# Kernel tuning notes

Hardware: AMD Instinct MI355X
Metric: run time of the kernel (lower is better)

## Reference

```python
import jax, jax.numpy as jnp
import numpy as np

B = 262144
NUM_PLAYERS = 450
EMBED = 8


def _lin(x, w, b):
    return x @ w + b


def setup_inputs() -> dict:
    key = jax.random.key(0)
    ks = jax.random.split(key, 32)
    # state: 73 continuous features + 5 player ids stored as floats
    cont = jax.random.normal(ks[0], (B, 73), dtype=jnp.float32)
    pids = jax.random.randint(ks[1], (B, 5), 0, NUM_PLAYERS).astype(jnp.float32)
    state = jnp.concatenate([cont, pids], axis=1)

    def w(k, shape, fan_in):
        return jax.random.normal(k, shape, dtype=jnp.float32) * (2.0 / fan_in) ** 0.5

    base_in = 13 + EMBED + 32      # ctx(21) + pooled defender phi(32) = 53
    pass_in = 32 + base_in         # tm_phi(32) + base(53) = 85? no: 32+53=85 -> wait
    pass_in = 32 + (13 + EMBED) + 32  # tm_phi + ctx + def_pooled = 32+21+32 = 85
    # Match torch: pass_input = 32 + ctx_dim + 32 where ctx_dim = 13+embed = 21 -> 85?
    # torch: ctx_dim = 13 + embed_dim = 21; base_input = ctx_dim + 32 = 53; pass_input = 32 + ctx_dim + 32 = 85.
    # BUT forward concatenates [tm_phi, ctx, def_pooled] = 32 + 21 + 32 = 85. Consistent.
    pass_in = 85
    return {
        "state": state,
        "emb": jax.random.normal(ks[2], (NUM_PLAYERS, EMBED), dtype=jnp.float32),
        "wd1": w(ks[3], (4, 32), 4),   "bd1": jnp.zeros((32,), jnp.float32),
        "wd2": w(ks[4], (32, 32), 32), "bd2": jnp.zeros((32,), jnp.float32),
        "wt1": w(ks[5], (10 + EMBED, 32), 18), "bt1": jnp.zeros((32,), jnp.float32),
        "wt2": w(ks[6], (32, 32), 32),         "bt2": jnp.zeros((32,), jnp.float32),
        "wv1": w(ks[7], (base_in, 64), base_in), "bv1": jnp.zeros((64,), jnp.float32),
        "wv2": w(ks[8], (64, 32), 64),           "bv2": jnp.zeros((32,), jnp.float32),
        "wv3": w(ks[9], (32, 1), 32),            "bv3": jnp.zeros((1,), jnp.float32),
        "ws1": w(ks[10], (base_in, 32), base_in), "bs1": jnp.zeros((32,), jnp.float32),
        "ws2": w(ks[11], (32, 1), 32),            "bs2": jnp.zeros((1,), jnp.float32),
        "wp1": w(ks[12], (pass_in, 64), pass_in), "bp1": jnp.zeros((64,), jnp.float32),
        "wp2": w(ks[13], (64, 16), 64),           "bp2": jnp.zeros((16,), jnp.float32),
        "wp3": w(ks[14], (16, 1), 16),            "bp3": jnp.zeros((1,), jnp.float32),
    }


def reference(state, emb, wd1, bd1, wd2, bd2, wt1, bt1, wt2, bt2,
              wv1, bv1, wv2, bv2, wv3, bv3, ws1, bs1, ws2, bs2,
              wp1, bp1, wp2, bp2, wp3, bp3):
    b = state.shape[0]
    context = state[:, :11]
    tm_open = state[:, 11:15]
    tm_fg = state[:, 15:19]
    tm_dist = state[:, 19:23]
    def_pos = state[:, 23:33].reshape(b, 5, 2)
    tm_pos = state[:, 33:41].reshape(b, 4, 2)
    bh_vel = state[:, 41:43]
    def_vel = state[:, 43:53].reshape(b, 5, 2)
    tm_vel = state[:, 53:61].reshape(b, 4, 2)
    tm_lane_min = state[:, 61:65]
    tm_corridor = state[:, 65:69]
    tm_pass_dist = state[:, 69:73]

    pids = jnp.clip(state[:, 73:78].astype(jnp.int32), 0, NUM_PLAYERS - 1)
    bh_embed = emb[pids[:, 0]]            # [b, E]
    tm_embeds = emb[pids[:, 1:5]]         # [b, 4, E]

    # batched defender phi over 5 entities: [b,5,4] -> [b,5,32]
    d_feat = jnp.concatenate([def_pos, def_vel], axis=-1)
    d_h = jax.nn.relu(jax.nn.relu(d_feat @ wd1 + bd1) @ wd2 + bd2)
    def_pooled = d_h.mean(axis=1)         # [b, 32]

    ctx = jnp.concatenate([context, bh_vel, bh_embed], axis=1)   # [b, 21]
    base = jnp.concatenate([ctx, def_pooled], axis=1)            # [b, 53]

    value = jax.nn.relu(jax.nn.relu(base @ wv1 + bv1) @ wv2 + bv2) @ wv3 + bv3  # [b,1]
    a_shoot = jax.nn.relu(base @ ws1 + bs1) @ ws2 + bs2                          # [b,1]

    # batched teammate phi over 4 entities: [b,4,18] -> [b,4,32]
    t_feat = jnp.concatenate([
        tm_pos, tm_vel,
        tm_open[:, :, None], tm_fg[:, :, None], tm_dist[:, :, None],
        tm_lane_min[:, :, None], tm_corridor[:, :, None], tm_pass_dist[:, :, None],
        tm_embeds,
    ], axis=-1)
    tm_phi = jax.nn.relu(jax.nn.relu(t_feat @ wt1 + bt1) @ wt2 + bt2)  # [b,4,32]

    base_b = jnp.broadcast_to(base[:, None, :], (b, 4, base.shape[1]))
    p_in = jnp.concatenate([tm_phi, base_b], axis=-1)                   # [b,4,85]
    a_pass = (jax.nn.relu(jax.nn.relu(p_in @ wp1 + bp1) @ wp2 + bp2) @ wp3 + bp3)[..., 0]  # [b,4]
    a_pass = a_pass - a_pass.mean(axis=1, keepdims=True)

    q_shoot = value + a_shoot          # [b,1]
    q_passes = value + a_pass          # [b,4]
    return jnp.concatenate([q_shoot, q_passes], axis=1)
```

## Files before the change

kernel.cpp:

```cpp
#include <hip/hip_runtime.h>
#include <hip/hip_bf16.h>

#define THREADS 512

typedef short bf16x8 __attribute__((ext_vector_type(8)));
typedef float f32x4 __attribute__((ext_vector_type(4)));

union FragU { unsigned u[4]; bf16x8 v; };

__device__ __forceinline__ void split8(const float* x, FragU& hi, FragU& lo) {
#pragma unroll
    for (int i = 0; i < 4; ++i) {
        float a = x[2 * i], b = x[2 * i + 1];
        __hip_bfloat162 h2 = __float22bfloat162_rn(make_float2(a, b));
        float ra = __bfloat162float(h2.x), rb = __bfloat162float(h2.y);
        __hip_bfloat162 l2 = __float22bfloat162_rn(make_float2(a - ra, b - rb));
        unsigned hu, lu;
        __builtin_memcpy(&hu, &h2, 4);
        __builtin_memcpy(&lu, &l2, 4);
        hi.u[i] = hu; lo.u[i] = lu;
    }
}

__device__ __forceinline__ f32x4 mm3(const FragU& ah, const FragU& al,
                                     const FragU& bh, const FragU& bl, f32x4 acc) {
    acc = __builtin_amdgcn_mfma_f32_16x16x32_bf16(al.v, bh.v, acc, 0, 0, 0);
    acc = __builtin_amdgcn_mfma_f32_16x16x32_bf16(ah.v, bl.v, acc, 0, 0, 0);
    acc = __builtin_amdgcn_mfma_f32_16x16x32_bf16(ah.v, bh.v, acc, 0, 0, 0);
    return acc;
}

__device__ __forceinline__ void load_pair(const uint4* __restrict__ ws, int pair, int lane,
                                          FragU& hi, FragU& lo) {
    uint4 a = ws[pair * 128 + lane];
    uint4 b = ws[pair * 128 + 64 + lane];
    hi.u[0] = a.x; hi.u[1] = a.y; hi.u[2] = a.z; hi.u[3] = a.w;
    lo.u[0] = b.x; lo.u[1] = b.y; lo.u[2] = b.z; lo.u[3] = b.w;
}

__device__ __forceinline__ void buildA(const float* buf, int stride, int m, int kf, int lane,
                                       FragU& hi, FragU& lo) {
    const float* p = buf + (m * 16 + (lane & 15)) * stride + kf * 32 + ((lane >> 4) * 8);
    float x[8];
    *reinterpret_cast<float4*>(&x[0]) = *reinterpret_cast<const float4*>(p);
    *reinterpret_cast<float4*>(&x[4]) = *reinterpret_cast<const float4*>(p + 4);
    split8(x, hi, lo);
}

__device__ __forceinline__ void storeC(float* buf, int stride, int m, int nf, int lane, f32x4 c) {
    float* p = buf + (((lane >> 4) * 4) + m * 16) * stride + nf * 16 + (lane & 15);
    p[0] = c[0]; p[stride] = c[1]; p[2 * stride] = c[2]; p[3 * stride] = c[3];
}

#define PB_D2  0
#define PB_T1  2
#define PB_T2  4
#define PB_P1T 6
#define PB_P1B 10
#define PB_P2  18
#define PB_V1  20
#define PB_V2  28
#define PB_S1  32
#define WS_BYTES (36 * 2048)

__global__ __launch_bounds__(64)
void prep_weights(const float* __restrict__ wd2, const float* __restrict__ wt1,
                  const float* __restrict__ wt2, const float* __restrict__ wp1,
                  const float* __restrict__ wp2, const float* __restrict__ wv1,
                  const float* __restrict__ wv2, const float* __restrict__ ws1,
                  uint4* __restrict__ wsout) {
    const int pair = blockIdx.x;
    const int lane = threadIdx.x;
    const int base_[10]  = {0, 2, 4, 6, 10, 18, 20, 28, 32, 36};
    const int kreal_[9]  = {32, 18, 32, 32, 53, 64, 53, 64, 53};
    const int n_[9]      = {32, 32, 32, 64, 64, 16, 64, 32, 32};
    const int nfc_[9]    = {2, 2, 2, 4, 4, 1, 4, 2, 2};
    const int roff_[9]   = {0, 0, 0, 0, 32, 0, 0, 0, 0};
    int g = 0;
    while (g < 8 && pair >= base_[g + 1]) ++g;
    const int local = pair - base_[g];
    const int kf = local / nfc_[g];
    const int nfi = local % nfc_[g];
    const float* W = (g == 0) ? wd2 : (g == 1) ? wt1 : (g == 2) ? wt2 :
                     (g == 3 || g == 4) ? wp1 : (g == 5) ? wp2 :
                     (g == 6) ? wv1 : (g == 7) ? wv2 : ws1;
    const int N = n_[g];
    float x[8];
#pragma unroll
    for (int j = 0; j < 8; ++j) {
        const int k = kf * 32 + (lane >> 4) * 8 + j;
        const int n = nfi * 16 + (lane & 15);
        x[j] = (k < kreal_[g]) ? W[(roff_[g] + k) * N + n] : 0.0f;
    }
    FragU hi, lo;
    split8(x, hi, lo);
    wsout[pair * 128 + lane]      = make_uint4(hi.u[0], hi.u[1], hi.u[2], hi.u[3]);
    wsout[pair * 128 + 64 + lane] = make_uint4(lo.u[0], lo.u[1], lo.u[2], lo.u[3]);
}

#define SB 68
#define SS 36
#define WAVE_F 4608

__global__ __launch_bounds__(THREADS, 2)
void dueling_mfma(const float* __restrict__ state, const float* __restrict__ emb,
                  const float* __restrict__ wd1, const float* __restrict__ bd1,
                  const float* __restrict__ bd2, const float* __restrict__ bt1,
                  const float* __restrict__ bt2, const float* __restrict__ bv1,
                  const float* __restrict__ bv2, const float* __restrict__ wv3,
                  const float* __restrict__ bv3, const float* __restrict__ bs1,
                  const float* __restrict__ ws2, const float* __restrict__ bs2,
                  const float* __restrict__ bp1, const float* __restrict__ bp2,
                  const float* __restrict__ wp3,
                  const uint4* __restrict__ ws, float* __restrict__ out, int nrows) {
    __shared__ float smem[8 * WAVE_F];
    const int lane = threadIdx.x & 63;
    const int wave = threadIdx.x >> 6;
    const int row = blockIdx.x * THREADS + wave * 64 + lane;
    const float* __restrict__ s = state + (long long)row * 78;

    float* BASE = smem + wave * WAVE_F;
    float* BUFA = BASE;
    float* BUFB = BASE + 64 * SS;
    float* HST  = BASE + 24;
    const int c16 = lane & 15;

#pragma unroll
    for (int i = 0; i < 17; ++i)
        *reinterpret_cast<float4*>(BASE + lane * SB + i * 4) = make_float4(0.f, 0.f, 0.f, 0.f);

    {
        int pid0 = (int)s[73];
        pid0 = pid0 < 0 ? 0 : (pid0 > 449 ? 449 : pid0);
        const float4 e0 = *(const float4*)(emb + pid0 * 8);
        const float4 e1 = *(const float4*)(emb + pid0 * 8 + 4);
        float* bp = BASE + lane * SB;
        *reinterpret_cast<float4*>(bp +  0) = make_float4(s[0], s[1], s[2], s[3]);
        *reinterpret_cast<float4*>(bp +  4) = make_float4(s[4], s[5], s[6], s[7]);
        *reinterpret_cast<float4*>(bp +  8) = make_float4(s[8], s[9], s[10], s[41]);
        *reinterpret_cast<float4*>(bp + 12) = make_float4(s[42], e0.x, e0.y, e0.z);
        *reinterpret_cast<float4*>(bp + 16) = make_float4(e0.w, e1.x, e1.y, e1.z);
        bp[20] = e1.w;
    }

    float pool[4][2][4];
#pragma unroll
    for (int m = 0; m < 4; ++m)
#pragma unroll
        for (int nf = 0; nf < 2; ++nf)
#pragma unroll
            for (int q = 0; q < 4; ++q) pool[m][nf][q] = 0.0f;

#pragma unroll 1
    for (int p = 0; p < 5; ++p) {
        const float f0 = s[23 + 2 * p], f1 = s[24 + 2 * p];
        const float f2 = s[43 + 2 * p], f3 = s[44 + 2 * p];
#pragma unroll
        for (int i = 0; i < 8; ++i) {
            const float4 b4 = *(const float4*)(bd1 + i * 4);
            const float4 w0 = *(const float4*)(wd1 + 0 * 32 + i * 4);
            const float4 w1 = *(const float4*)(wd1 + 1 * 32 + i * 4);
            const float4 w2 = *(const float4*)(wd1 + 2 * 32 + i * 4);
            const float4 w3 = *(const float4*)(wd1 + 3 * 32 + i * 4);
            float4 hv;
            hv.x = fmaxf(fmaf(f0, w0.x, fmaf(f1, w1.x, fmaf(f2, w2.x, fmaf(f3, w3.x, b4.x)))), 0.f);
            hv.y = fmaxf(fmaf(f0, w0.y, fmaf(f1, w1.y, fmaf(f2, w2.y, fmaf(f3, w3.y, b4.y)))), 0.f);
            hv.z = fmaxf(fmaf(f0, w0.z, fmaf(f1, w1.z, fmaf(f2, w2.z, fmaf(f3, w3.z, b4.z)))), 0.f);
            hv.w = fmaxf(fmaf(f0, w0.w, fmaf(f1, w1.w, fmaf(f2, w2.w, fmaf(f3, w3.w, b4.w)))), 0.f);
            *reinterpret_cast<float4*>(BASE + lane * SB + 24 + i * 4) = hv;
        }

        FragU ah[4], al[4];
#pragma unroll
        for (int m = 0; m < 4; ++m) buildA(HST, SB, m, 0, lane, ah[m], al[m]);
#pragma unroll
        for (int nf = 0; nf < 2; ++nf) {
            FragU bh, bl; load_pair(ws, PB_D2 + nf, lane, bh, bl);
            const float bias = bd2[nf * 16 + c16];
#pragma unroll
            for (int m = 0; m < 4; ++m) {
                f32x4 acc = {bias, bias, bias, bias};
                acc = mm3(ah[m], al[m], bh, bl, acc);
#pragma unroll
                for (int q = 0; q < 4; ++q) pool[m][nf][q] += fmaxf(acc[q], 0.0f);
            }
        }
    }
    BASE[lane * SB + 53] = 0.0f;
    BASE[lane * SB + 54] = 0.0f;
    BASE[lane * SB + 55] = 0.0f;
#pragma unroll
    for (int m = 0; m < 4; ++m)
#pragma unroll
        for (int nf = 0; nf < 2; ++nf)
#pragma unroll
            for (int q = 0; q < 4; ++q)
                BASE[((lane >> 4) * 4 + q + m * 16) * SB + 21 + nf * 16 + c16] =
                    pool[m][nf][q] * 0.2f;

    FragU Xh[4][2], Xl[4][2];
#pragma unroll
    for (int m = 0; m < 4; ++m)
#pragma unroll
        for (int kf = 0; kf < 2; ++kf)
            buildA(BASE, SB, m, kf, lane, Xh[m][kf], Xl[m][kf]);

    float v2acc[4][2][4];
#pragma unroll
    for (int m = 0; m < 4; ++m)
#pragma unroll
        for (int nf = 0; nf < 2; ++nf) {
            const float b = bv2[nf * 16 + c16];
#pragma unroll
            for (int q = 0; q < 4; ++q) v2acc[m][nf][q] = b;
        }
#pragma unroll 1
    for (int half = 0; half < 2; ++half) {
#pragma unroll
        for (int nfl = 0; nfl < 2; ++nfl) {
            const int ng = half * 2 + nfl;
            FragU b0h, b0l, b1h, b1l;
            load_pair(ws, PB_V1 + ng, lane, b0h, b0l);
            load_pair(ws, PB_V1 + 4 + ng, lane, b1h, b1l);
            const float bias = bv1[ng * 16 + c16];
#pragma unroll
            for (int m = 0; m < 4; ++m) {
                f32x4 acc = {bias, bias, bias, bias};
                acc = mm3(Xh[m][0], Xl[m][0], b0h, b0l, acc);
                acc = mm3(Xh[m][1], Xl[m][1], b1h, b1l, acc);
#pragma unroll
                for (int q = 0; q < 4; ++q) acc[q] = fmaxf(acc[q], 0.0f);
                storeC(BUFA, SS, m, nfl, lane, acc);
            }
        }
        FragU ah[4], al[4];
#pragma unroll
        for (int m = 0; m < 4; ++m) buildA(BUFA, SS, m, 0, lane, ah[m], al[m]);
#pragma unroll
        for (int nf = 0; nf < 2; ++nf) {
            FragU bh, bl; load_pair(ws, PB_V2 + half * 2 + nf, lane, bh, bl);
#pragma unroll
            for (int m = 0; m < 4; ++m) {
                f32x4 acc = {v2acc[m][nf][0], v2acc[m][nf][1], v2acc[m][nf][2], v2acc[m][nf][3]};
                acc = mm3(ah[m], al[m], bh, bl, acc);
#pragma unroll
                for (int q = 0; q < 4; ++q) v2acc[m][nf][q] = acc[q];
            }
        }
    }
#pragma unroll
    for (int m = 0; m < 4; ++m)
#pragma unroll
        for (int nf = 0; nf < 2; ++nf) {
            f32x4 r = {fmaxf(v2acc[m][nf][0], 0.f), fmaxf(v2acc[m][nf][1], 0.f),
                       fmaxf(v2acc[m][nf][2], 0.f), fmaxf(v2acc[m][nf][3], 0.f)};
            storeC(BUFA, SS, m, nf, lane, r);
        }
    float value = bv3[0];
#pragma unroll
    for (int c4 = 0; c4 < 8; ++c4) {
        float4 v = *reinterpret_cast<const float4*>(BUFA + lane * SS + c4 * 4);
        value = fmaf(v.x, wv3[c4 * 4], value);
        value = fmaf(v.y, wv3[c4 * 4 + 1], value);
        value = fmaf(v.z, wv3[c4 * 4 + 2], value);
        value = fmaf(v.w, wv3[c4 * 4 + 3], value);
    }

#pragma unroll
    for (int nf = 0; nf < 2; ++nf) {
        FragU b0h, b0l, b1h, b1l;
        load_pair(ws, PB_S1 + nf, lane, b0h, b0l);
        load_pair(ws, PB_S1 + 2 + nf, lane, b1h, b1l);
        const float bias = bs1[nf * 16 + c16];
#pragma unroll
        for (int m = 0; m < 4; ++m) {
            f32x4 acc = {bias, bias, bias, bias};
            acc = mm3(Xh[m][0], Xl[m][0], b0h, b0l, acc);
            acc = mm3(Xh[m][1], Xl[m][1], b1h, b1l, acc);
#pragma unroll
            for (int q = 0; q < 4; ++q) acc[q] = fmaxf(acc[q], 0.0f);
            storeC(BUFA, SS, m, nf, lane, acc);
        }
    }
    float ashoot = bs2[0];
#pragma unroll
    for (int c4 = 0; c4 < 8; ++c4) {
        float4 v = *reinterpret_cast<const float4*>(BUFA + lane * SS + c4 * 4);
        ashoot = fmaf(v.x, ws2[c4 * 4], ashoot);
        ashoot = fmaf(v.y, ws2[c4 * 4 + 1], ashoot);
        ashoot = fmaf(v.z, ws2[c4 * 4 + 2], ashoot);
        ashoot = fmaf(v.w, ws2[c4 * 4 + 3], ashoot);
    }

    float ap0 = 0.f, ap1 = 0.f, ap2 = 0.f, ap3 = 0.f;
#pragma unroll 1
    for (int j = 0; j < 4; ++j) {
        {
            int pid = (int)s[74 + j];
            pid = pid < 0 ? 0 : (pid > 449 ? 449 : pid);
            const float4 e0 = *(const float4*)(emb + pid * 8);
            const float4 e1 = *(const float4*)(emb + pid * 8 + 4);
            float* tp = BUFA + lane * SS;
            *reinterpret_cast<float4*>(tp +  0) =
                make_float4(s[33 + 2 * j], s[34 + 2 * j], s[53 + 2 * j], s[54 + 2 * j]);
            *reinterpret_cast<float4*>(tp +  4) =
                make_float4(s[11 + j], s[15 + j], s[19 + j], s[61 + j]);
            *reinterpret_cast<float4*>(tp +  8) = make_float4(s[65 + j], s[69 + j], e0.x, e0.y);
            *reinterpret_cast<float4*>(tp + 12) = make_float4(e0.z, e0.w, e1.x, e1.y);
            *reinterpret_cast<float4*>(tp + 16) = make_float4(e1.z, e1.w, 0.f, 0.f);
            *reinterpret_cast<float4*>(tp + 20) = make_float4(0.f, 0.f, 0.f, 0.f);
            *reinterpret_cast<float4*>(tp + 24) = make_float4(0.f, 0.f, 0.f, 0.f);
            *reinterpret_cast<float4*>(tp + 28) = make_float4(0.f, 0.f, 0.f, 0.f);
        }
        {
            FragU ah[4], al[4];
#pragma unroll
            for (int m = 0; m < 4; ++m) buildA(BUFA, SS, m, 0, lane, ah[m], al[m]);
#pragma unroll
            for (int nf = 0; nf < 2; ++nf) {
                FragU bh, bl; load_pair(ws, PB_T1 + nf, lane, bh, bl);
                const float bias = bt1[nf * 16 + c16];
#pragma unroll
                for (int m = 0; m < 4; ++m) {
                    f32x4 acc = {bias, bias, bias, bias};
                    acc = mm3(ah[m], al[m], bh, bl, acc);
#pragma unroll
                    for (int q = 0; q < 4; ++q) acc[q] = fmaxf(acc[q], 0.0f);
                    storeC(BUFB, SS, m, nf, lane, acc);
                }
            }
        }
        {
            FragU ah[4], al[4];
#pragma unroll
            for (int m = 0; m < 4; ++m) buildA(BUFB, SS, m, 0, lane, ah[m], al[m]);
#pragma unroll
            for (int nf = 0; nf < 2; ++nf) {
                FragU bh, bl; load_pair(ws, PB_T2 + nf, lane, bh, bl);
                const float bias = bt2[nf * 16 + c16];
#pragma unroll
                for (int m = 0; m < 4; ++m) {
                    f32x4 acc = {bias, bias, bias, bias};
                    acc = mm3(ah[m], al[m], bh, bl, acc);
#pragma unroll
                    for (int q = 0; q < 4; ++q) acc[q] = fmaxf(acc[q], 0.0f);
                    storeC(BUFA, SS, m, nf, lane, acc);
                }
            }
        }
        FragU th[4], tl[4];
#pragma unroll
        for (int m = 0; m < 4; ++m) buildA(BUFA, SS, m, 0, lane, th[m], tl[m]);

        float p2acc[4][4];
        {
            const float b = bp2[c16];
#pragma unroll
            for (int m = 0; m < 4; ++m)
#pragma unroll
                for (int q = 0; q < 4; ++q) p2acc[m][q] = b;
        }
#pragma unroll 1
        for (int half = 0; half < 2; ++half) {
#pragma unroll
            for (int nfl = 0; nfl < 2; ++nfl) {
                const int ng = half * 2 + nfl;
                FragU bth, btl, b0h, b0l, b1h, b1l;
                load_pair(ws, PB_P1T + ng, lane, bth, btl);
                load_pair(ws, PB_P1B + ng, lane, b0h, b0l);
                load_pair(ws, PB_P1B + 4 + ng, lane, b1h, b1l);
                const float bias = bp1[ng * 16 + c16];
#pragma unroll
                for (int m = 0; m < 4; ++m) {
                    f32x4 acc = {bias, bias, bias, bias};
                    acc = mm3(th[m], tl[m], bth, btl, acc);
                    acc = mm3(Xh[m][0], Xl[m][0], b0h, b0l, acc);
                    acc = mm3(Xh[m][1], Xl[m][1], b1h, b1l, acc);
#pragma unroll
                    for (int q = 0; q < 4; ++q) acc[q] = fmaxf(acc[q], 0.0f);
                    storeC(BUFB, SS, m, nfl, lane, acc);
                }
            }
            FragU ah[4], al[4];
#pragma unroll
            for (int m = 0; m < 4; ++m) buildA(BUFB, SS, m, 0, lane, ah[m], al[m]);
            FragU bh, bl; load_pair(ws, PB_P2 + half, lane, bh, bl);
#pragma unroll
            for (int m = 0; m < 4; ++m) {
                f32x4 acc = {p2acc[m][0], p2acc[m][1], p2acc[m][2], p2acc[m][3]};
                acc = mm3(ah[m], al[m], bh, bl, acc);
#pragma unroll
                for (int q = 0; q < 4; ++q) p2acc[m][q] = acc[q];
            }
        }
#pragma unroll
        for (int m = 0; m < 4; ++m) {
            f32x4 r = {fmaxf(p2acc[m][0], 0.f), fmaxf(p2acc[m][1], 0.f),
                       fmaxf(p2acc[m][2], 0.f), fmaxf(p2acc[m][3], 0.f)};
            storeC(BUFB, SS, m, 0, lane, r);
        }
        float ap = 0.0f;
#pragma unroll
        for (int c4 = 0; c4 < 4; ++c4) {
            float4 v = *reinterpret_cast<const float4*>(BUFB + lane * SS + c4 * 4);
            ap = fmaf(v.x, wp3[c4 * 4], ap);
            ap = fmaf(v.y, wp3[c4 * 4 + 1], ap);
            ap = fmaf(v.z, wp3[c4 * 4 + 2], ap);
            ap = fmaf(v.w, wp3[c4 * 4 + 3], ap);
        }
        if (j == 0) ap0 = ap;
        else if (j == 1) ap1 = ap;
        else if (j == 2) ap2 = ap;
        else ap3 = ap;
    }

    const float am = 0.25f * (ap0 + ap1 + ap2 + ap3);
    float* __restrict__ o = out + (long long)row * 5;
    o[0] = value + ashoot;
    o[1] = value + ap0 - am;
    o[2] = value + ap1 - am;
    o[3] = value + ap2 - am;
    o[4] = value + ap3 - am;
}

__global__ __launch_bounds__(256)
void dueling_fwd_valu(const float* __restrict__ state, const float* __restrict__ emb,
                      const float* __restrict__ wd1, const float* __restrict__ bd1,
                      const float* __restrict__ wd2, const float* __restrict__ bd2,
                      const float* __restrict__ wt1, const float* __restrict__ bt1,
                      const float* __restrict__ wt2, const float* __restrict__ bt2,
                      const float* __restrict__ wv1, const float* __restrict__ bv1,
                      const float* __restrict__ wv2, const float* __restrict__ bv2,
                      const float* __restrict__ wv3, const float* __restrict__ bv3,
                      const float* __restrict__ ws1, const float* __restrict__ bs1,
                      const float* __restrict__ ws2, const float* __restrict__ bs2,
                      const float* __restrict__ wp1, const float* __restrict__ bp1,
                      const float* __restrict__ wp2, const float* __restrict__ bp2,
                      const float* __restrict__ wp3, const float* __restrict__ bp3,
                      float* __restrict__ out, int nrows) {
    const int row = blockIdx.x * 256 + threadIdx.x;
    if (row >= nrows) return;
    const float* __restrict__ s = state + (long long)row * 78;
    float def_pooled[32];
#pragma unroll
    for (int n = 0; n < 32; ++n) def_pooled[n] = 0.0f;
#pragma unroll 1
    for (int p = 0; p < 5; ++p) {
        const float f0 = s[23 + 2 * p], f1 = s[24 + 2 * p], f2 = s[43 + 2 * p], f3 = s[44 + 2 * p];
        float h1[32];
#pragma unroll
        for (int n = 0; n < 32; ++n) {
            float a = bd1[n];
            a = fmaf(f0, wd1[n], a); a = fmaf(f1, wd1[32 + n], a);
            a = fmaf(f2, wd1[64 + n], a); a = fmaf(f3, wd1[96 + n], a);
            h1[n] = fmaxf(a, 0.0f);
        }
        float a2[32];
#pragma unroll
        for (int n = 0; n < 32; ++n) a2[n] = bd2[n];
#pragma unroll
        for (int k = 0; k < 32; ++k) {
            const float hk = h1[k];
#pragma unroll
            for (int n = 0; n < 32; ++n) a2[n] = fmaf(hk, wd2[k * 32 + n], a2[n]);
        }
#pragma unroll
        for (int n = 0; n < 32; ++n) def_pooled[n] += fmaxf(a2[n], 0.0f);
    }
    float base[53];
#pragma unroll
    for (int i = 0; i < 11; ++i) base[i] = s[i];
    base[11] = s[41]; base[12] = s[42];
    {
        int pid0 = (int)s[73];
        pid0 = pid0 < 0 ? 0 : (pid0 > 449 ? 449 : pid0);
        const float4 e0 = *(const float4*)(emb + pid0 * 8);
        const float4 e1 = *(const float4*)(emb + pid0 * 8 + 4);
        base[13] = e0.x; base[14] = e0.y; base[15] = e0.z; base[16] = e0.w;
        base[17] = e1.x; base[18] = e1.y; base[19] = e1.z; base[20] = e1.w;
    }
#pragma unroll
    for (int n = 0; n < 32; ++n) base[21 + n] = def_pooled[n] * 0.2f;
    float a_shoot;
    {
        float t[32];
#pragma unroll
        for (int n = 0; n < 32; ++n) t[n] = bs1[n];
#pragma unroll
        for (int k = 0; k < 53; ++k) {
            const float xk = base[k];
#pragma unroll
            for (int n = 0; n < 32; ++n) t[n] = fmaf(xk, ws1[k * 32 + n], t[n]);
        }
        a_shoot = bs2[0];
#pragma unroll
        for (int k = 0; k < 32; ++k) a_shoot = fmaf(fmaxf(t[k], 0.0f), ws2[k], a_shoot);
    }
    float value;
    {
        float h32[32];
#pragma unroll
        for (int n = 0; n < 32; ++n) h32[n] = bv2[n];
#pragma unroll
        for (int half = 0; half < 2; ++half) {
            float hh[32];
#pragma unroll
            for (int n = 0; n < 32; ++n) hh[n] = bv1[half * 32 + n];
#pragma unroll
            for (int k = 0; k < 53; ++k) {
                const float xk = base[k];
#pragma unroll
                for (int n = 0; n < 32; ++n) hh[n] = fmaf(xk, wv1[k * 64 + half * 32 + n], hh[n]);
            }
#pragma unroll
            for (int k = 0; k < 32; ++k) {
                const float xk = fmaxf(hh[k], 0.0f);
#pragma unroll
                for (int n = 0; n < 32; ++n) h32[n] = fmaf(xk, wv2[(half * 32 + k) * 32 + n], h32[n]);
            }
        }
        value = bv3[0];
#pragma unroll
        for (int k = 0; k < 32; ++k) value = fmaf(fmaxf(h32[k], 0.0f), wv3[k], value);
    }
    float pb[64];
#pragma unroll
    for (int n = 0; n < 64; ++n) pb[n] = bp1[n];
#pragma unroll
    for (int k = 0; k < 53; ++k) {
        const float xk = base[k];
#pragma unroll
        for (int n = 0; n < 64; ++n) pb[n] = fmaf(xk, wp1[(32 + k) * 64 + n], pb[n]);
    }
    float ap0 = 0.f, ap1 = 0.f, ap2 = 0.f, ap3 = 0.f;
#pragma unroll 1
    for (int j = 0; j < 4; ++j) {
        float t1[32];
        {
            float tf[18];
            tf[0] = s[33 + 2 * j]; tf[1] = s[34 + 2 * j];
            tf[2] = s[53 + 2 * j]; tf[3] = s[54 + 2 * j];
            tf[4] = s[11 + j]; tf[5] = s[15 + j]; tf[6] = s[19 + j];
            tf[7] = s[61 + j]; tf[8] = s[65 + j]; tf[9] = s[69 + j];
            int pid = (int)s[74 + j];
            pid = pid < 0 ? 0 : (pid > 449 ? 449 : pid);
            const float4 e0 = *(const float4*)(emb + pid * 8);
            const float4 e1 = *(const float4*)(emb + pid * 8 + 4);
            tf[10] = e0.x; tf[11] = e0.y; tf[12] = e0.z; tf[13] = e0.w;
            tf[14] = e1.x; tf[15] = e1.y; tf[16] = e1.z; tf[17] = e1.w;
#pragma unroll
            for (int n = 0; n < 32; ++n) t1[n] = bt1[n];
#pragma unroll
            for (int k = 0; k < 18; ++k) {
                const float xk = tf[k];
#pragma unroll
                for (int n = 0; n < 32; ++n) t1[n] = fmaf(xk, wt1[k * 32 + n], t1[n]);
            }
        }
        float t2[32];
#pragma unroll
        for (int n = 0; n < 32; ++n) t2[n] = bt2[n];
#pragma unroll
        for (int k = 0; k < 32; ++k) {
            const float xk = fmaxf(t1[k], 0.0f);
#pragma unroll
            for (int n = 0; n < 32; ++n) t2[n] = fmaf(xk, wt2[k * 32 + n], t2[n]);
        }
#pragma unroll
        for (int n = 0; n < 32; ++n) t2[n] = fmaxf(t2[n], 0.0f);
        float p2[16];
#pragma unroll
        for (int n = 0; n < 16; ++n) p2[n] = bp2[n];
#pragma unroll
        for (int half = 0; half < 2; ++half) {
            float phh[32];
#pragma unroll
            for (int n = 0; n < 32; ++n) phh[n] = pb[half * 32 + n];
#pragma unroll
            for (int k = 0; k < 32; ++k) {
                const float xk = t2[k];
#pragma unroll
                for (int n = 0; n < 32; ++n) phh[n] = fmaf(xk, wp1[k * 64 + half * 32 + n], phh[n]);
            }
#pragma unroll
            for (int k = 0; k < 32; ++k) {
                const float xk = fmaxf(phh[k], 0.0f);
#pragma unroll
                for (int n = 0; n < 16; ++n) p2[n] = fmaf(xk, wp2[(half * 32 + k) * 16 + n], p2[n]);
            }
        }
        float a = bp3[0];
#pragma unroll
        for (int k = 0; k < 16; ++k) a = fmaf(fmaxf(p2[k], 0.0f), wp3[k], a);
        if (j == 0) ap0 = a; else if (j == 1) ap1 = a; else if (j == 2) ap2 = a; else ap3 = a;
    }
    const float am = 0.25f * (ap0 + ap1 + ap2 + ap3);
    float* __restrict__ o = out + (long long)row * 5;
    o[0] = value + a_shoot;
    o[1] = value + ap0 - am;
    o[2] = value + ap1 - am;
    o[3] = value + ap2 - am;
    o[4] = value + ap3 - am;
}

extern "C" void kernel_launch(void* const* d_in, const int* in_sizes, int n_in,
                              void* d_out, int out_size, void* d_ws, size_t ws_size,
                              hipStream_t stream) {
    const float* state = (const float*)d_in[0];
    const float* emb   = (const float*)d_in[1];
    const float* wd1 = (const float*)d_in[2];  const float* bd1 = (const float*)d_in[3];
    const float* wd2 = (const float*)d_in[4];  const float* bd2 = (const float*)d_in[5];
    const float* wt1 = (const float*)d_in[6];  const float* bt1 = (const float*)d_in[7];
    const float* wt2 = (const float*)d_in[8];  const float* bt2 = (const float*)d_in[9];
    const float* wv1 = (const float*)d_in[10]; const float* bv1 = (const float*)d_in[11];
    const float* wv2 = (const float*)d_in[12]; const float* bv2 = (const float*)d_in[13];
    const float* wv3 = (const float*)d_in[14]; const float* bv3 = (const float*)d_in[15];
    const float* ws1 = (const float*)d_in[16]; const float* bs1 = (const float*)d_in[17];
    const float* ws2 = (const float*)d_in[18]; const float* bs2 = (const float*)d_in[19];
    const float* wp1 = (const float*)d_in[20]; const float* bp1 = (const float*)d_in[21];
    const float* wp2 = (const float*)d_in[22]; const float* bp2 = (const float*)d_in[23];
    const float* wp3 = (const float*)d_in[24]; const float* bp3 = (const float*)d_in[25];

    const int nrows = in_sizes[0] / 78;

    if (ws_size < (size_t)WS_BYTES || (nrows & (THREADS - 1)) != 0) {
        const int blocks = (nrows + 255) / 256;
        dueling_fwd_valu<<<blocks, 256, 0, stream>>>(
            state, emb, wd1, bd1, wd2, bd2, wt1, bt1, wt2, bt2,
            wv1, bv1, wv2, bv2, wv3, bv3, ws1, bs1, ws2, bs2,
            wp1, bp1, wp2, bp2, wp3, bp3, (float*)d_out, nrows);
        return;
    }

    prep_weights<<<36, 64, 0, stream>>>(wd2, wt1, wt2, wp1, wp2, wv1, wv2, ws1,
                                        (uint4*)d_ws);
    dueling_mfma<<<nrows / THREADS, THREADS, 0, stream>>>(
        state, emb, wd1, bd1, bd2, bt1, bt2, bv1, bv2, wv3, bv3,
        bs1, ws2, bs2, bp1, bp2, wp3,
        (const uint4*)d_ws, (float*)d_out, nrows);
}
```

Baseline: 155.1 us.

## Process 32 rows per wave instead of 64 to cut registers and LDS

Each wave now handles 32 rows (two MFMA M-tiles instead of four), with the two half-waves splitting the first-layer defender VALU work and only the lower half doing row-level loads and output writes. The goal is to halve per-wave LDS and accumulator and fragment registers, allowing more resident waves and better latency hiding. The cost is a doubled grid, duplicated weight-fragment loads per row, and idle half-wave lanes in the scalar parts of the kernel.

```diff
diff --git a/kernel.cpp b/kernel.cpp
--- a/kernel.cpp
+++ b/kernel.cpp
@@ -100,9 +100,9 @@
 
 #define SB 68
 #define SS 36
-#define WAVE_F 4608
-
-__global__ __launch_bounds__(THREADS, 2)
+#define WAVE_F 2304
+
+__global__ __launch_bounds__(THREADS)
 void dueling_mfma(const float* __restrict__ state, const float* __restrict__ emb,
                   const float* __restrict__ wd1, const float* __restrict__ bd1,
                   const float* __restrict__ bd2, const float* __restrict__ bt1,
@@ -116,25 +116,27 @@
     __shared__ float smem[8 * WAVE_F];
     const int lane = threadIdx.x & 63;
     const int wave = threadIdx.x >> 6;
-    const int row = blockIdx.x * THREADS + wave * 64 + lane;
+    const int r    = lane & 31;
+    const int sub  = lane >> 5;
+    const int row  = blockIdx.x * 256 + wave * 32 + r;
     const float* __restrict__ s = state + (long long)row * 78;
 
     float* BASE = smem + wave * WAVE_F;
     float* BUFA = BASE;
-    float* BUFB = BASE + 64 * SS;
+    float* BUFB = BASE + 32 * SS;
     float* HST  = BASE + 24;
     const int c16 = lane & 15;
 
 #pragma unroll
-    for (int i = 0; i < 17; ++i)
-        *reinterpret_cast<float4*>(BASE + lane * SB + i * 4) = make_float4(0.f, 0.f, 0.f, 0.f);
-
-    {
+    for (int i = 0; i < 9; ++i)
+        *reinterpret_cast<float4*>(BASE + i * 256 + lane * 4) = make_float4(0.f, 0.f, 0.f, 0.f);
+
+    if (lane < 32) {
         int pid0 = (int)s[73];
         pid0 = pid0 < 0 ? 0 : (pid0 > 449 ? 449 : pid0);
         const float4 e0 = *(const float4*)(emb + pid0 * 8);
         const float4 e1 = *(const float4*)(emb + pid0 * 8 + 4);
-        float* bp = BASE + lane * SB;
+        float* bp = BASE + r * SB;
         *reinterpret_cast<float4*>(bp +  0) = make_float4(s[0], s[1], s[2], s[3]);
         *reinterpret_cast<float4*>(bp +  4) = make_float4(s[4], s[5], s[6], s[7]);
         *reinterpret_cast<float4*>(bp +  8) = make_float4(s[8], s[9], s[10], s[41]);
@@ -143,9 +145,9 @@
         bp[20] = e1.w;
     }
 
-    float pool[4][2][4];
-#pragma unroll
-    for (int m = 0; m < 4; ++m)
+    float pool[2][2][4];
+#pragma unroll
+    for (int m = 0; m < 2; ++m)
 #pragma unroll
         for (int nf = 0; nf < 2; ++nf)
 #pragma unroll
@@ -156,7 +158,8 @@
         const float f0 = s[23 + 2 * p], f1 = s[24 + 2 * p];
         const float f2 = s[43 + 2 * p], f3 = s[44 + 2 * p];
 #pragma unroll
-        for (int i = 0; i < 8; ++i) {
+        for (int i2 = 0; i2 < 4; ++i2) {
+            const int i = sub * 4 + i2;
             const float4 b4 = *(const float4*)(bd1 + i * 4);
             const float4 w0 = *(const float4*)(wd1 + 0 * 32 + i * 4);
             const float4 w1 = *(const float4*)(wd1 + 1 * 32 + i * 4);
@@ -167,18 +170,18 @@
             hv.y = fmaxf(fmaf(f0, w0.y, fmaf(f1, w1.y, fmaf(f2, w2.y, fmaf(f3, w3.y, b4.y)))), 0.f);
             hv.z = fmaxf(fmaf(f0, w0.z, fmaf(f1, w1.z, fmaf(f2, w2.z, fmaf(f3, w3.z, b4.z)))), 0.f);
             hv.w = fmaxf(fmaf(f0, w0.w, fmaf(f1, w1.w, fmaf(f2, w2.w, fmaf(f3, w3.w, b4.w)))), 0.f);
-            *reinterpret_cast<float4*>(BASE + lane * SB + 24 + i * 4) = hv;
-        }
-
-        FragU ah[4], al[4];
-#pragma unroll
-        for (int m = 0; m < 4; ++m) buildA(HST, SB, m, 0, lane, ah[m], al[m]);
+            *reinterpret_cast<float4*>(BASE + r * SB + 24 + i * 4) = hv;
+        }
+
+        FragU ah[2], al[2];
+#pragma unroll
+        for (int m = 0; m < 2; ++m) buildA(HST, SB, m, 0, lane, ah[m], al[m]);
 #pragma unroll
         for (int nf = 0; nf < 2; ++nf) {
             FragU bh, bl; load_pair(ws, PB_D2 + nf, lane, bh, bl);
             const float bias = bd2[nf * 16 + c16];
 #pragma unroll
-            for (int m = 0; m < 4; ++m) {
+            for (int m = 0; m < 2; ++m) {
                 f32x4 acc = {bias, bias, bias, bias};
                 acc = mm3(ah[m], al[m], bh, bl, acc);
 #pragma unroll
@@ -186,11 +189,11 @@
             }
         }
     }
-    BASE[lane * SB + 53] = 0.0f;
-    BASE[lane * SB + 54] = 0.0f;
-    BASE[lane * SB + 55] = 0.0f;
-#pragma unroll
-    for (int m = 0; m < 4; ++m)
+    BASE[r * SB + 53] = 0.0f;
+    BASE[r * SB + 54] = 0.0f;
+    BASE[r * SB + 55] = 0.0f;
+#pragma unroll
+    for (int m = 0; m < 2; ++m)
 #pragma unroll
         for (int nf = 0; nf < 2; ++nf)
 #pragma unroll
@@ -198,16 +201,16 @@
                 BASE[((lane >> 4) * 4 + q + m * 16) * SB + 21 + nf * 16 + c16] =
                     pool[m][nf][q] * 0.2f;
 
-    FragU Xh[4][2], Xl[4][2];
-#pragma unroll
-    for (int m = 0; m < 4; ++m)
+    FragU Xh[2][2], Xl[2][2];
+#pragma unroll
+    for (int m = 0; m < 2; ++m)
 #pragma unroll
         for (int kf = 0; kf < 2; ++kf)
             buildA(BASE, SB, m, kf, lane, Xh[m][kf], Xl[m][kf]);
 
-    float v2acc[4][2][4];
-#pragma unroll
-    for (int m = 0; m < 4; ++m)
+    float v2acc[2][2][4];
+#pragma unroll
+    for (int m = 0; m < 2; ++m)
 #pragma unroll
         for (int nf = 0; nf < 2; ++nf) {
             const float b = bv2[nf * 16 + c16];
@@ -224,7 +227,7 @@
             load_pair(ws, PB_V1 + 4 + ng, lane, b1h, b1l);
             const float bias = bv1[ng * 16 + c16];
 #pragma unroll
-            for (int m = 0; m < 4; ++m) {
+            for (int m = 0; m < 2; ++m) {
                 f32x4 acc = {bias, bias, bias, bias};
                 acc = mm3(Xh[m][0], Xl[m][0], b0h, b0l, acc);
                 acc = mm3(Xh[m][1], Xl[m][1], b1h, b1l, acc);
@@ -233,14 +236,14 @@
                 storeC(BUFA, SS, m, nfl, lane, acc);
             }
         }
-        FragU ah[4], al[4];
-#pragma unroll
-        for (int m = 0; m < 4; ++m) buildA(BUFA, SS, m, 0, lane, ah[m], al[m]);
+        FragU ah[2], al[2];
+#pragma unroll
+        for (int m = 0; m < 2; ++m) buildA(BUFA, SS, m, 0, lane, ah[m], al[m]);
 #pragma unroll
         for (int nf = 0; nf < 2; ++nf) {
             FragU bh, bl; load_pair(ws, PB_V2 + half * 2 + nf, lane, bh, bl);
 #pragma unroll
-            for (int m = 0; m < 4; ++m) {
+            for (int m = 0; m < 2; ++m) {
                 f32x4 acc = {v2acc[m][nf][0], v2acc[m][nf][1], v2acc[m][nf][2], v2acc[m][nf][3]};
                 acc = mm3(ah[m], al[m], bh, bl, acc);
 #pragma unroll
@@ -249,17 +252,17 @@
         }
     }
 #pragma unroll
-    for (int m = 0; m < 4; ++m)
+    for (int m = 0; m < 2; ++m)
 #pragma unroll
         for (int nf = 0; nf < 2; ++nf) {
-            f32x4 r = {fmaxf(v2acc[m][nf][0], 0.f), fmaxf(v2acc[m][nf][1], 0.f),
-                       fmaxf(v2acc[m][nf][2], 0.f), fmaxf(v2acc[m][nf][3], 0.f)};
-            storeC(BUFA, SS, m, nf, lane, r);
+            f32x4 rr = {fmaxf(v2acc[m][nf][0], 0.f), fmaxf(v2acc[m][nf][1], 0.f),
+                        fmaxf(v2acc[m][nf][2], 0.f), fmaxf(v2acc[m][nf][3], 0.f)};
+            storeC(BUFA, SS, m, nf, lane, rr);
         }
     float value = bv3[0];
 #pragma unroll
     for (int c4 = 0; c4 < 8; ++c4) {
-        float4 v = *reinterpret_cast<const float4*>(BUFA + lane * SS + c4 * 4);
+        float4 v = *reinterpret_cast<const float4*>(BUFA + r * SS + c4 * 4);
         value = fmaf(v.x, wv3[c4 * 4], value);
         value = fmaf(v.y, wv3[c4 * 4 + 1], value);
         value = fmaf(v.z, wv3[c4 * 4 + 2], value);
@@ -273,7 +276,7 @@
         load_pair(ws, PB_S1 + 2 + nf, lane, b1h, b1l);
         const float bias = bs1[nf * 16 + c16];
 #pragma unroll
-        for (int m = 0; m < 4; ++m) {
+        for (int m = 0; m < 2; ++m) {
             f32x4 acc = {bias, bias, bias, bias};
             acc = mm3(Xh[m][0], Xl[m][0], b0h, b0l, acc);
             acc = mm3(Xh[m][1], Xl[m][1], b1h, b1l, acc);
@@ -285,7 +288,7 @@
     float ashoot = bs2[0];
 #pragma unroll
     for (int c4 = 0; c4 < 8; ++c4) {
-        float4 v = *reinterpret_cast<const float4*>(BUFA + lane * SS + c4 * 4);
+        float4 v = *reinterpret_cast<const float4*>(BUFA + r * SS + c4 * 4);
         ashoot = fmaf(v.x, ws2[c4 * 4], ashoot);
         ashoot = fmaf(v.y, ws2[c4 * 4 + 1], ashoot);
         ashoot = fmaf(v.z, ws2[c4 * 4 + 2], ashoot);
@@ -295,12 +298,12 @@
     float ap0 = 0.f, ap1 = 0.f, ap2 = 0.f, ap3 = 0.f;
 #pragma unroll 1
     for (int j = 0; j < 4; ++j) {
-        {
+        if (lane < 32) {
             int pid = (int)s[74 + j];
             pid = pid < 0 ? 0 : (pid > 449 ? 449 : pid);
             const float4 e0 = *(const float4*)(emb + pid * 8);
             const float4 e1 = *(const float4*)(emb + pid * 8 + 4);
-            float* tp = BUFA + lane * SS;
+            float* tp = BUFA + r * SS;
             *reinterpret_cast<float4*>(tp +  0) =
                 make_float4(s[33 + 2 * j], s[34 + 2 * j], s[53 + 2 * j], s[54 + 2 * j]);
             *reinterpret_cast<float4*>(tp +  4) =
@@ -313,15 +316,15 @@
             *reinterpret_cast<float4*>(tp + 28) = make_float4(0.f, 0.f, 0.f, 0.f);
         }
         {
-            FragU ah[4], al[4];
-#pragma unroll
-            for (int m = 0; m < 4; ++m) buildA(BUFA, SS, m, 0, lane, ah[m], al[m]);
+            FragU ah[2], al[2];
+#pragma unroll
+            for (int m = 0; m < 2; ++m) buildA(BUFA, SS, m, 0, lane, ah[m], al[m]);
 #pragma unroll
             for (int nf = 0; nf < 2; ++nf) {
                 FragU bh, bl; load_pair(ws, PB_T1 + nf, lane, bh, bl);
                 const float bias = bt1[nf * 16 + c16];
 #pragma unroll
-                for (int m = 0; m < 4; ++m) {
+                for (int m = 0; m < 2; ++m) {
                     f32x4 acc = {bias, bias, bias, bias};
                     acc = mm3(ah[m], al[m], bh, bl, acc);
 #pragma unroll
@@ -331,15 +334,15 @@
             }
         }
         {
-            FragU ah[4], al[4];
-#pragma unroll
-            for (int m = 0; m < 4; ++m) buildA(BUFB, SS, m, 0, lane, ah[m], al[m]);
+            FragU ah[2], al[2];
+#pragma unroll
+            for (int m = 0; m < 2; ++m) buildA(BUFB, SS, m, 0, lane, ah[m], al[m]);
 #pragma unroll
             for (int nf = 0; nf < 2; ++nf) {
                 FragU bh, bl; load_pair(ws, PB_T2 + nf, lane, bh, bl);
                 const float bias = bt2[nf * 16 + c16];
 #pragma unroll
-                for (int m = 0; m < 4; ++m) {
+                for (int m = 0; m < 2; ++m) {
                     f32x4 acc = {bias, bias, bias, bias};
                     acc = mm3(ah[m], al[m], bh, bl, acc);
 #pragma unroll
@@ -348,15 +351,15 @@
                 }
             }
         }
-        FragU th[4], tl[4];
-#pragma unroll
-        for (int m = 0; m < 4; ++m) buildA(BUFA, SS, m, 0, lane, th[m], tl[m]);
-
-        float p2acc[4][4];
+        FragU th[2], tl[2];
+#pragma unroll
+        for (int m = 0; m < 2; ++m) buildA(BUFA, SS, m, 0, lane, th[m], tl[m]);
+
+        float p2acc[2][4];
         {
             const float b = bp2[c16];
 #pragma unroll
-            for (int m = 0; m < 4; ++m)
+            for (int m = 0; m < 2; ++m)
 #pragma unroll
                 for (int q = 0; q < 4; ++q) p2acc[m][q] = b;
         }
@@ -371,7 +374,7 @@
                 load_pair(ws, PB_P1B + 4 + ng, lane, b1h, b1l);
                 const float bias = bp1[ng * 16 + c16];
 #pragma unroll
-                for (int m = 0; m < 4; ++m) {
+                for (int m = 0; m < 2; ++m) {
                     f32x4 acc = {bias, bias, bias, bias};
                     acc = mm3(th[m], tl[m], bth, btl, acc);
                     acc = mm3(Xh[m][0], Xl[m][0], b0h, b0l, acc);
@@ -381,12 +384,12 @@
                     storeC(BUFB, SS, m, nfl, lane, acc);
                 }
             }
-            FragU ah[4], al[4];
-#pragma unroll
-            for (int m = 0; m < 4; ++m) buildA(BUFB, SS, m, 0, lane, ah[m], al[m]);
+            FragU ah[2], al[2];
+#pragma unroll
+            for (int m = 0; m < 2; ++m) buildA(BUFB, SS, m, 0, lane, ah[m], al[m]);
             FragU bh, bl; load_pair(ws, PB_P2 + half, lane, bh, bl);
 #pragma unroll
-            for (int m = 0; m < 4; ++m) {
+            for (int m = 0; m < 2; ++m) {
                 f32x4 acc = {p2acc[m][0], p2acc[m][1], p2acc[m][2], p2acc[m][3]};
                 acc = mm3(ah[m], al[m], bh, bl, acc);
 #pragma unroll
@@ -394,15 +397,15 @@
             }
         }
 #pragma unroll
-        for (int m = 0; m < 4; ++m) {
-            f32x4 r = {fmaxf(p2acc[m][0], 0.f), fmaxf(p2acc[m][1], 0.f),
-                       fmaxf(p2acc[m][2], 0.f), fmaxf(p2acc[m][3], 0.f)};
-            storeC(BUFB, SS, m, 0, lane, r);
+        for (int m = 0; m < 2; ++m) {
+            f32x4 rr = {fmaxf(p2acc[m][0], 0.f), fmaxf(p2acc[m][1], 0.f),
+                        fmaxf(p2acc[m][2], 0.f), fmaxf(p2acc[m][3], 0.f)};
+            storeC(BUFB, SS, m, 0, lane, rr);
         }
         float ap = 0.0f;
 #pragma unroll
         for (int c4 = 0; c4 < 4; ++c4) {
-            float4 v = *reinterpret_cast<const float4*>(BUFB + lane * SS + c4 * 4);
+            float4 v = *reinterpret_cast<const float4*>(BUFB + r * SS + c4 * 4);
             ap = fmaf(v.x, wp3[c4 * 4], ap);
             ap = fmaf(v.y, wp3[c4 * 4 + 1], ap);
             ap = fmaf(v.z, wp3[c4 * 4 + 2], ap);
@@ -414,13 +417,15 @@
         else ap3 = ap;
     }
 
-    const float am = 0.25f * (ap0 + ap1 + ap2 + ap3);
-    float* __restrict__ o = out + (long long)row * 5;
-    o[0] = value + ashoot;
-    o[1] = value + ap0 - am;
-    o[2] = value + ap1 - am;
-    o[3] = value + ap2 - am;
-    o[4] = value + ap3 - am;
+    if (lane < 32) {
+        const float am = 0.25f * (ap0 + ap1 + ap2 + ap3);
+        float* __restrict__ o = out + (long long)row * 5;
+        o[0] = value + ashoot;
+        o[1] = value + ap0 - am;
+        o[2] = value + ap1 - am;
+        o[3] = value + ap2 - am;
+        o[4] = value + ap3 - am;
+    }
 }
 
 __global__ __launch_bounds__(256)
@@ -623,7 +628,7 @@
 
     const int nrows = in_sizes[0] / 78;
 
-    if (ws_size < (size_t)WS_BYTES || (nrows & (THREADS - 1)) != 0) {
+    if (ws_size < (size_t)WS_BYTES || (nrows & 255) != 0) {
         const int blocks = (nrows + 255) / 256;
         dueling_fwd_valu<<<blocks, 256, 0, stream>>>(
             state, emb, wd1, bd1, wd2, bd2, wt1, bt1, wt2, bt2,
@@ -634,7 +639,7 @@
 
     prep_weights<<<36, 64, 0, stream>>>(wd2, wt1, wt2, wp1, wp2, wv1, wv2, ws1,
                                         (uint4*)d_ws);
-    dueling_mfma<<<nrows / THREADS, THREADS, 0, stream>>>(
+    dueling_mfma<<<nrows / 256, THREADS, 0, stream>>>(
         state, emb, wd1, bd1, bd2, bt1, bt2, bv1, bv2, wv3, bv3,
         bs1, ws2, bs2, bp1, bp2, wp3,
         (const uint4*)d_ws, (float*)d_out, nrows);
```

Result: faster. 128.0 us (-17.5%).
